# Optimization experiments

Measured on AMD Instinct MI355X. Metric: run time of the kernel, lower is better.

## Reference

```python
import jax, jax.numpy as jnp
import numpy as np

B, LQ, LK, D, H = 8, 1024, 1024, 1024, 16
HD = D // H  # 64


def setup_inputs() -> dict:
    key = jax.random.key(0)
    ks = jax.random.split(key, 8)
    s = 0.02  # weight init scale
    return {
        "q_in": jax.random.normal(ks[0], (B, LQ, D), jnp.float32),
        "k_in": jax.random.normal(ks[1], (B, LK, D), jnp.float32),
        "v_in": jax.random.normal(ks[2], (B, LK, D), jnp.float32),
        "wq": jax.random.normal(ks[3], (D, D), jnp.float32) * s,
        "bq": jnp.zeros((D,), jnp.float32),
        "wk": jax.random.normal(ks[4], (D, D), jnp.float32) * s,
        "bk": jnp.zeros((D,), jnp.float32),
        "wv": jax.random.normal(ks[5], (D, D), jnp.float32) * s,
        "bv": jnp.zeros((D,), jnp.float32),
        "wo": jax.random.normal(ks[6], (D, D), jnp.float32) * s,
        "bo": jnp.zeros((D,), jnp.float32),
        # is_masked=True buffer: tril of ones -> True on lower triangle (masked-out positions, per original masked_fill semantics)
        "mask": jnp.tril(jnp.ones((LQ, LK), jnp.bool_)),
    }


def reference(q_in, k_in, v_in, wq, bq, wk, bk, wv, bv, wo, bo, mask):
    # torch Linear: x @ W.T + b
    q = (q_in @ wq.T + bq).reshape(B, H, LQ, HD)  # plain view, as in original
    k = (k_in @ wk.T + bk).reshape(B, H, LK, HD)
    v = (v_in @ wv.T + bv).reshape(B, H, LK, HD)
    # QUIRK: original scales by sqrt(query.size(1)) == sqrt(head_num), not sqrt(head_dim)
    scale = jnp.sqrt(jnp.float32(H))
    h = jnp.einsum("bhik,bhjk->bhij", q, k) / scale  # [B,H,LQ,LK]
    # masked_fill(-inf) then nan_to_num (maps -inf -> finfo.min, matching torch defaults)
    h = jnp.nan_to_num(jnp.where(mask, -jnp.inf, h))
    w = jax.nn.softmax(h, axis=-1)
    heads = jnp.einsum("bhij,bhjv->bhiv", w, v).reshape(B, LQ, H * HD)
    return heads @ wo.T + bo
```

## Files before the change

kernel.cpp:

```cpp
#include <hip/hip_runtime.h>
#include <hip/hip_bf16.h>

typedef __bf16 bf16;
typedef __attribute__((ext_vector_type(8))) __bf16 bf16x8;
typedef __attribute__((ext_vector_type(4))) float f32x4;

#define BB 8
#define SEQ 1024
#define DD 1024
#define HDIM 64
#define CHUNK 65536
#define MROWS (BB * SEQ)
#define NE_IN 8388608
#define NE_W  1048576

__device__ __forceinline__ void async_load16(const bf16* g, bf16* l) {
  __builtin_amdgcn_global_load_lds(
      (const __attribute__((address_space(1))) void*)g,
      (__attribute__((address_space(3))) void*)l, 16, 0, 0);
}

struct CvtArgs {
  const float* src[7];
  bf16* dst[7];
  int n[7];
};
__global__ __launch_bounds__(256) void cvt_bf16(CvtArgs a) {
  const int t = blockIdx.y;
  const long idx = ((long)blockIdx.x * 256 + threadIdx.x) * 8;
  if (idx >= a.n[t]) return;
  const float* s = a.src[t] + idx;
  f32x4 x = *(const f32x4*)s;
  f32x4 y = *(const f32x4*)(s + 4);
  bf16x8 o;
  o[0] = (bf16)x[0]; o[1] = (bf16)x[1]; o[2] = (bf16)x[2]; o[3] = (bf16)x[3];
  o[4] = (bf16)y[0]; o[5] = (bf16)y[1]; o[6] = (bf16)y[2]; o[7] = (bf16)y[3];
  *(bf16x8*)(a.dst[t] + idx) = o;
}

__global__ __launch_bounds__(256) void gemm_qkv(
    const bf16* __restrict__ Abase, const bf16* __restrict__ Wbase,
    const float* __restrict__ bq, const float* __restrict__ bk,
    const float* __restrict__ bv, bf16* __restrict__ Obase)
{
  __shared__ __attribute__((aligned(16))) bf16 As[128 * 32];
  __shared__ __attribute__((aligned(16))) bf16 Bs[128 * 32];

  const int tid  = threadIdx.x;
  const int lane = tid & 63;
  const int wid  = tid >> 6;
  const int wm   = wid >> 1, wn = wid & 1;
  const int quad = lane >> 4, l15 = lane & 15;
  const int m0 = blockIdx.y * 128;
  const int n0 = blockIdx.x * 128;
  const int t  = n0 >> 10;

  const bf16* A = Abase + (size_t)t * NE_IN;
  const float* bias = (t == 0) ? bq : (t == 1) ? bk : bv;
  const float scale = (t == 0) ? 0.25f : 1.0f;
  bf16* Cout = Obase + (size_t)t * NE_IN;
  const int nc0 = n0 & 1023;

  f32x4 acc[4][4];
#pragma unroll
  for (int i = 0; i < 4; i++)
#pragma unroll
    for (int j = 0; j < 4; j++) acc[i][j] = f32x4{0.f, 0.f, 0.f, 0.f};

  const int srow = wid * 16 + (lane >> 2);
  const int scol = (lane & 3) * 8;
  const bf16* gA = A + (size_t)(m0 + srow) * DD + scol;
  const bf16* gB = Wbase + (size_t)(n0 + srow) * DD + scol;
  bf16* lA = As + wid * 512;
  bf16* lB = Bs + wid * 512;

  for (int k0 = 0; k0 < DD; k0 += 32) {
    async_load16(gA + k0,           lA);
    async_load16(gA + k0 + 64 * DD, lA + 2048);
    async_load16(gB + k0,           lB);
    async_load16(gB + k0 + 64 * DD, lB + 2048);
    __syncthreads();

    bf16x8 af[4], bfr[4];
#pragma unroll
    for (int mi = 0; mi < 4; mi++)
      af[mi] = *(const bf16x8*)&As[(wm * 64 + mi * 16 + l15) * 32 + quad * 8];
#pragma unroll
    for (int ni = 0; ni < 4; ni++)
      bfr[ni] = *(const bf16x8*)&Bs[(wn * 64 + ni * 16 + l15) * 32 + quad * 8];
#pragma unroll
    for (int mi = 0; mi < 4; mi++)
#pragma unroll
      for (int ni = 0; ni < 4; ni++)
        acc[mi][ni] = __builtin_amdgcn_mfma_f32_16x16x32_bf16(
            af[mi], bfr[ni], acc[mi][ni], 0, 0, 0);
    __syncthreads();
  }

#pragma unroll
  for (int mi = 0; mi < 4; mi++) {
#pragma unroll
    for (int ni = 0; ni < 4; ni++) {
      const int col = nc0 + wn * 64 + ni * 16 + l15;
      const float bv_ = bias[col];
#pragma unroll
      for (int r = 0; r < 4; r++) {
        const int row = m0 + wm * 64 + mi * 16 + quad * 4 + r;
        Cout[(size_t)row * DD + col] = (bf16)((acc[mi][ni][r] + bv_) * scale);
      }
    }
  }
}

__global__ __launch_bounds__(256) void gemm_out(
    const bf16* __restrict__ A, const bf16* __restrict__ Bw,
    const float* __restrict__ bias, float* __restrict__ Cout)
{
  __shared__ __attribute__((aligned(16))) bf16 As[128 * 32];
  __shared__ __attribute__((aligned(16))) bf16 Bs[128 * 32];

  const int tid  = threadIdx.x;
  const int lane = tid & 63;
  const int wid  = tid >> 6;
  const int wm   = wid >> 1, wn = wid & 1;
  const int quad = lane >> 4, l15 = lane & 15;
  const int m0 = blockIdx.y * 128;
  const int n0 = blockIdx.x * 128;

  f32x4 acc[4][4];
#pragma unroll
  for (int i = 0; i < 4; i++)
#pragma unroll
    for (int j = 0; j < 4; j++) acc[i][j] = f32x4{0.f, 0.f, 0.f, 0.f};

  const int srow = wid * 16 + (lane >> 2);
  const int scol = (lane & 3) * 8;
  const bf16* gA = A  + (size_t)(m0 + srow) * DD + scol;
  const bf16* gB = Bw + (size_t)(n0 + srow) * DD + scol;
  bf16* lA = As + wid * 512;
  bf16* lB = Bs + wid * 512;

  for (int k0 = 0; k0 < DD; k0 += 32) {
    async_load16(gA + k0,           lA);
    async_load16(gA + k0 + 64 * DD, lA + 2048);
    async_load16(gB + k0,           lB);
    async_load16(gB + k0 + 64 * DD, lB + 2048);
    __syncthreads();

    bf16x8 af[4], bfr[4];
#pragma unroll
    for (int mi = 0; mi < 4; mi++)
      af[mi] = *(const bf16x8*)&As[(wm * 64 + mi * 16 + l15) * 32 + quad * 8];
#pragma unroll
    for (int ni = 0; ni < 4; ni++)
      bfr[ni] = *(const bf16x8*)&Bs[(wn * 64 + ni * 16 + l15) * 32 + quad * 8];
#pragma unroll
    for (int mi = 0; mi < 4; mi++)
#pragma unroll
      for (int ni = 0; ni < 4; ni++)
        acc[mi][ni] = __builtin_amdgcn_mfma_f32_16x16x32_bf16(
            af[mi], bfr[ni], acc[mi][ni], 0, 0, 0);
    __syncthreads();
  }

#pragma unroll
  for (int mi = 0; mi < 4; mi++) {
#pragma unroll
    for (int ni = 0; ni < 4; ni++) {
      const int col = n0 + wn * 64 + ni * 16 + l15;
      const float bv_ = bias[col];
#pragma unroll
      for (int r = 0; r < 4; r++) {
        const int row = m0 + wm * 64 + mi * 16 + quad * 4 + r;
        Cout[(size_t)row * DD + col] = acc[mi][ni][r] + bv_;
      }
    }
  }
}

__global__ __launch_bounds__(256) void vtrans(
    const bf16* __restrict__ V, bf16* __restrict__ Vt)
{
  __shared__ __attribute__((aligned(16))) bf16 T[64][72];
  const int tid = threadIdx.x;
  const int r  = tid >> 2;
  const int c0 = (tid & 3) * 16;
  const size_t base = (size_t)blockIdx.y * CHUNK;
  const int kv0 = blockIdx.x * 64;

  const bf16* src = V + base + (size_t)(kv0 + r) * HDIM + c0;
  *(bf16x8*)&T[r][c0]     = *(const bf16x8*)src;
  *(bf16x8*)&T[r][c0 + 8] = *(const bf16x8*)(src + 8);
  __syncthreads();

  bf16x8 o0, o1;
#pragma unroll
  for (int j = 0; j < 8; j++) { o0[j] = T[c0 + j][r]; o1[j] = T[c0 + 8 + j][r]; }
  bf16* dst = Vt + base + (size_t)r * SEQ + kv0 + c0;
  *(bf16x8*)dst       = o0;
  *(bf16x8*)(dst + 8) = o1;
}

__global__ __launch_bounds__(256) void attn3(
    const bf16* __restrict__ Q, const bf16* __restrict__ K,
    const bf16* __restrict__ Vt, bf16* __restrict__ O)
{
  __shared__ __attribute__((aligned(16))) bf16 Ks[64][72];
  __shared__ __attribute__((aligned(16))) bf16 Vs[64][72];
  __shared__ __attribute__((aligned(16))) bf16 Ps[4][16][72];

  const int tid  = threadIdx.x;
  const int lane = tid & 63;
  const int wid  = tid >> 6;
  const int quad = lane >> 4, l15 = lane & 15;
  const int q0   = blockIdx.y * 64;
  const size_t base = (size_t)blockIdx.x * CHUNK;
  const int qrow0 = q0 + wid * 16;
  const int rowq  = qrow0 + quad * 4;

  bf16x8 qa[2];
#pragma unroll
  for (int ks = 0; ks < 2; ks++)
    qa[ks] = *(const bf16x8*)&Q[base + (size_t)(qrow0 + l15) * HDIM + ks * 32 + quad * 8];

  f32x4 oacc[4];
  float lsum[4] = {0.f, 0.f, 0.f, 0.f};
#pragma unroll
  for (int t = 0; t < 4; t++) oacc[t] = f32x4{0.f, 0.f, 0.f, 0.f};

  const int sr = tid >> 2;
  const int sc = (tid & 3) * 16;
  const bf16* gK = K  + base + (size_t)sr * HDIM + sc;
  const bf16* gV = Vt + base + (size_t)sr * SEQ  + sc;

  const int kv_begin = (q0 == SEQ - 64) ? 0 : q0;

  for (int kv0 = kv_begin; kv0 < SEQ; kv0 += 64) {
    {
      const bf16* pk = gK + (size_t)kv0 * HDIM;
      *(bf16x8*)&Ks[sr][sc]     = *(const bf16x8*)pk;
      *(bf16x8*)&Ks[sr][sc + 8] = *(const bf16x8*)(pk + 8);
      const bf16* pv = gV + kv0;
      *(bf16x8*)&Vs[sr][sc]     = *(const bf16x8*)pv;
      *(bf16x8*)&Vs[sr][sc + 8] = *(const bf16x8*)(pv + 8);
    }
    __syncthreads();

    f32x4 s[4];
#pragma unroll
    for (int ni = 0; ni < 4; ni++) {
      f32x4 a = f32x4{0.f, 0.f, 0.f, 0.f};
#pragma unroll
      for (int ks = 0; ks < 2; ks++) {
        bf16x8 kf = *(const bf16x8*)&Ks[ni * 16 + l15][ks * 32 + quad * 8];
        a = __builtin_amdgcn_mfma_f32_16x16x32_bf16(qa[ks], kf, a, 0, 0, 0);
      }
      s[ni] = a;
    }

#pragma unroll
    for (int ni = 0; ni < 4; ni++) {
      const int kvg = kv0 + ni * 16 + l15;
#pragma unroll
      for (int r = 0; r < 4; r++) {
        const int qg = rowq + r;
        float p;
        if (kvg <= qg) p = (qg == SEQ - 1) ? 1.0f : 0.0f;
        else           p = __expf(s[ni][r]);
        lsum[r] += p;
        Ps[wid][quad * 4 + r][ni * 16 + l15] = (bf16)p;
      }
    }

#pragma unroll
    for (int ks = 0; ks < 2; ks++) {
      bf16x8 pa = *(const bf16x8*)&Ps[wid][l15][ks * 32 + quad * 8];
#pragma unroll
      for (int t = 0; t < 4; t++) {
        bf16x8 vf = *(const bf16x8*)&Vs[t * 16 + l15][ks * 32 + quad * 8];
        oacc[t] = __builtin_amdgcn_mfma_f32_16x16x32_bf16(pa, vf, oacc[t], 0, 0, 0);
      }
    }
    __syncthreads();
  }

  float rinv[4];
#pragma unroll
  for (int r = 0; r < 4; r++) {
    float t = lsum[r];
#pragma unroll
    for (int off = 1; off < 16; off <<= 1) t += __shfl_xor(t, off);
    rinv[r] = 1.0f / t;
  }
#pragma unroll
  for (int t = 0; t < 4; t++)
#pragma unroll
    for (int r = 0; r < 4; r++)
      O[base + (size_t)(rowq + r) * HDIM + t * 16 + l15] = (bf16)(oacc[t][r] * rinv[r]);
}

extern "C" void kernel_launch(void* const* d_in, const int* in_sizes, int n_in,
                              void* d_out, int out_size, void* d_ws, size_t ws_size,
                              hipStream_t stream) {
  (void)in_sizes; (void)n_in; (void)out_size; (void)ws_size;
  const float* q_in = (const float*)d_in[0];
  const float* k_in = (const float*)d_in[1];
  const float* v_in = (const float*)d_in[2];
  const float* wq   = (const float*)d_in[3];
  const float* bq   = (const float*)d_in[4];
  const float* wk   = (const float*)d_in[5];
  const float* bk   = (const float*)d_in[6];
  const float* wv   = (const float*)d_in[7];
  const float* bv   = (const float*)d_in[8];
  const float* wo   = (const float*)d_in[9];
  const float* bo   = (const float*)d_in[10];

  bf16* wqb  = (bf16*)d_ws;
  bf16* wkb  = wqb + NE_W;
  bf16* wvb  = wkb + NE_W;
  bf16* wob  = wvb + NE_W;
  bf16* qinb = wob + NE_W;
  bf16* kinb = qinb + NE_IN;
  bf16* vinb = kinb + NE_IN;
  bf16* Qb   = vinb + NE_IN;
  bf16* Kb   = Qb + NE_IN;
  bf16* Vb   = Kb + NE_IN;
  bf16* VtG  = qinb;
  bf16* Hb   = kinb;

  CvtArgs ca;
  ca.src[0] = q_in; ca.dst[0] = qinb; ca.n[0] = NE_IN;
  ca.src[1] = k_in; ca.dst[1] = kinb; ca.n[1] = NE_IN;
  ca.src[2] = v_in; ca.dst[2] = vinb; ca.n[2] = NE_IN;
  ca.src[3] = wq;   ca.dst[3] = wqb;  ca.n[3] = NE_W;
  ca.src[4] = wk;   ca.dst[4] = wkb;  ca.n[4] = NE_W;
  ca.src[5] = wv;   ca.dst[5] = wvb;  ca.n[5] = NE_W;
  ca.src[6] = wo;   ca.dst[6] = wob;  ca.n[6] = NE_W;
  cvt_bf16<<<dim3(NE_IN / 2048, 7), 256, 0, stream>>>(ca);

  gemm_qkv<<<dim3(3 * DD / 128, MROWS / 128), 256, 0, stream>>>(
      qinb, wqb, bq, bk, bv, Qb);

  vtrans<<<dim3(SEQ / 64, BB * 16), 256, 0, stream>>>(Vb, VtG);
  attn3<<<dim3(BB * 16, SEQ / 64), 256, 0, stream>>>(Qb, Kb, VtG, Hb);

  gemm_out<<<dim3(DD / 128, MROWS / 128), 256, 0, stream>>>(
      Hb, wob, bo, (float*)d_out);
}
```

Measured before the change: 336.5 us.

## Keep attention probabilities in registers via transposed S and fp16 PV MFMA

The attention kernel now computes S transposed (K as the A operand), so each lane's score values line up directly as the B operand of a 16x16x16 fp16 MFMA for P·V. This removes the shared-memory round trip for P and the per-tile cross-lane row-sum reduction. V is stored transposed in fp16 to match, and the output is staged through shared memory for coalesced stores. Separately, the GEMM grid axes are swapped so blockIdx.x walks M tiles, which changes the tile traversal order and L2 reuse. fp16 P and V lower the accumulation precision somewhat, and PV now issues more, smaller MFMAs.

Measured after the change: 331.2 us. About the same (-1.6%).

```diff
diff --git a/kernel.cpp b/kernel.cpp
--- a/kernel.cpp
+++ b/kernel.cpp
@@ -2,7 +2,11 @@
 #include <hip/hip_bf16.h>
 
 typedef __bf16 bf16;
+typedef _Float16 f16;
 typedef __attribute__((ext_vector_type(8))) __bf16 bf16x8;
+typedef __attribute__((ext_vector_type(4))) __bf16 bf16x4;
+typedef __attribute__((ext_vector_type(8))) _Float16 f16x8;
+typedef __attribute__((ext_vector_type(4))) _Float16 f16x4;
 typedef __attribute__((ext_vector_type(4))) float f32x4;
 
 #define BB 8
@@ -51,8 +55,8 @@
   const int wid  = tid >> 6;
   const int wm   = wid >> 1, wn = wid & 1;
   const int quad = lane >> 4, l15 = lane & 15;
-  const int m0 = blockIdx.y * 128;
-  const int n0 = blockIdx.x * 128;
+  const int m0 = blockIdx.x * 128;
+  const int n0 = blockIdx.y * 128;
   const int t  = n0 >> 10;
 
   const bf16* A = Abase + (size_t)t * NE_IN;
@@ -124,8 +128,8 @@
   const int wid  = tid >> 6;
   const int wm   = wid >> 1, wn = wid & 1;
   const int quad = lane >> 4, l15 = lane & 15;
-  const int m0 = blockIdx.y * 128;
-  const int n0 = blockIdx.x * 128;
+  const int m0 = blockIdx.x * 128;
+  const int n0 = blockIdx.y * 128;
 
   f32x4 acc[4][4];
 #pragma unroll
@@ -179,7 +183,7 @@
 }
 
 __global__ __launch_bounds__(256) void vtrans(
-    const bf16* __restrict__ V, bf16* __restrict__ Vt)
+    const bf16* __restrict__ V, f16* __restrict__ Vt)
 {
   __shared__ __attribute__((aligned(16))) bf16 T[64][72];
   const int tid = threadIdx.x;
@@ -193,21 +197,23 @@
   *(bf16x8*)&T[r][c0 + 8] = *(const bf16x8*)(src + 8);
   __syncthreads();
 
-  bf16x8 o0, o1;
-#pragma unroll
-  for (int j = 0; j < 8; j++) { o0[j] = T[c0 + j][r]; o1[j] = T[c0 + 8 + j][r]; }
-  bf16* dst = Vt + base + (size_t)r * SEQ + kv0 + c0;
-  *(bf16x8*)dst       = o0;
-  *(bf16x8*)(dst + 8) = o1;
-}
-
-__global__ __launch_bounds__(256) void attn3(
+  f16x8 o0, o1;
+#pragma unroll
+  for (int j = 0; j < 8; j++) {
+    o0[j] = (f16)(float)T[c0 + j][r];
+    o1[j] = (f16)(float)T[c0 + 8 + j][r];
+  }
+  f16* dst = Vt + base + (size_t)r * SEQ + kv0 + c0;
+  *(f16x8*)dst       = o0;
+  *(f16x8*)(dst + 8) = o1;
+}
+
+__global__ __launch_bounds__(256) void attn5(
     const bf16* __restrict__ Q, const bf16* __restrict__ K,
-    const bf16* __restrict__ Vt, bf16* __restrict__ O)
+    const f16* __restrict__ Vt, bf16* __restrict__ O)
 {
   __shared__ __attribute__((aligned(16))) bf16 Ks[64][72];
-  __shared__ __attribute__((aligned(16))) bf16 Vs[64][72];
-  __shared__ __attribute__((aligned(16))) bf16 Ps[4][16][72];
+  __shared__ __attribute__((aligned(16))) f16  Vs[64][72];
 
   const int tid  = threadIdx.x;
   const int lane = tid & 63;
@@ -215,23 +221,22 @@
   const int quad = lane >> 4, l15 = lane & 15;
   const int q0   = blockIdx.y * 64;
   const size_t base = (size_t)blockIdx.x * CHUNK;
-  const int qrow0 = q0 + wid * 16;
-  const int rowq  = qrow0 + quad * 4;
-
-  bf16x8 qa[2];
+  const int qg = q0 + wid * 16 + l15;
+
+  bf16x8 qb[2];
 #pragma unroll
   for (int ks = 0; ks < 2; ks++)
-    qa[ks] = *(const bf16x8*)&Q[base + (size_t)(qrow0 + l15) * HDIM + ks * 32 + quad * 8];
+    qb[ks] = *(const bf16x8*)&Q[base + (size_t)qg * HDIM + ks * 32 + quad * 8];
 
   f32x4 oacc[4];
-  float lsum[4] = {0.f, 0.f, 0.f, 0.f};
-#pragma unroll
-  for (int t = 0; t < 4; t++) oacc[t] = f32x4{0.f, 0.f, 0.f, 0.f};
+#pragma unroll
+  for (int h = 0; h < 4; h++) oacc[h] = f32x4{0.f, 0.f, 0.f, 0.f};
+  float lsum = 0.f;
 
   const int sr = tid >> 2;
   const int sc = (tid & 3) * 16;
-  const bf16* gK = K  + base + (size_t)sr * HDIM + sc;
-  const bf16* gV = Vt + base + (size_t)sr * SEQ  + sc;
+  const bf16* gK = K + base + (size_t)sr * HDIM + sc;
+  const f16*  gV = Vt + base + (size_t)sr * SEQ + sc;
 
   const int kv_begin = (q0 == SEQ - 64) ? 0 : q0;
 
@@ -240,63 +245,59 @@
       const bf16* pk = gK + (size_t)kv0 * HDIM;
       *(bf16x8*)&Ks[sr][sc]     = *(const bf16x8*)pk;
       *(bf16x8*)&Ks[sr][sc + 8] = *(const bf16x8*)(pk + 8);
-      const bf16* pv = gV + kv0;
-      *(bf16x8*)&Vs[sr][sc]     = *(const bf16x8*)pv;
-      *(bf16x8*)&Vs[sr][sc + 8] = *(const bf16x8*)(pv + 8);
+      const f16* pv = gV + kv0;
+      *(f16x8*)&Vs[sr][sc]     = *(const f16x8*)pv;
+      *(f16x8*)&Vs[sr][sc + 8] = *(const f16x8*)(pv + 8);
     }
     __syncthreads();
 
-    f32x4 s[4];
-#pragma unroll
-    for (int ni = 0; ni < 4; ni++) {
-      f32x4 a = f32x4{0.f, 0.f, 0.f, 0.f};
+#pragma unroll
+    for (int t = 0; t < 4; t++) {
+      f32x4 s = f32x4{0.f, 0.f, 0.f, 0.f};
 #pragma unroll
       for (int ks = 0; ks < 2; ks++) {
-        bf16x8 kf = *(const bf16x8*)&Ks[ni * 16 + l15][ks * 32 + quad * 8];
-        a = __builtin_amdgcn_mfma_f32_16x16x32_bf16(qa[ks], kf, a, 0, 0, 0);
-      }
-      s[ni] = a;
-    }
-
-#pragma unroll
-    for (int ni = 0; ni < 4; ni++) {
-      const int kvg = kv0 + ni * 16 + l15;
+        bf16x8 kf = *(const bf16x8*)&Ks[t * 16 + l15][ks * 32 + quad * 8];
+        s = __builtin_amdgcn_mfma_f32_16x16x32_bf16(kf, qb[ks], s, 0, 0, 0);
+      }
+      f16x4 pf;
 #pragma unroll
       for (int r = 0; r < 4; r++) {
-        const int qg = rowq + r;
+        const int kvg = kv0 + t * 16 + quad * 4 + r;
         float p;
         if (kvg <= qg) p = (qg == SEQ - 1) ? 1.0f : 0.0f;
-        else           p = __expf(s[ni][r]);
-        lsum[r] += p;
-        Ps[wid][quad * 4 + r][ni * 16 + l15] = (bf16)p;
+        else           p = __expf(s[r]);
+        const f16 ph = (f16)p;
+        pf[r] = ph;
+        lsum += (float)ph;
+      }
+#pragma unroll
+      for (int h = 0; h < 4; h++) {
+        f16x4 vf = *(const f16x4*)&Vs[h * 16 + l15][t * 16 + quad * 4];
+        oacc[h] = __builtin_amdgcn_mfma_f32_16x16x16f16(vf, pf, oacc[h], 0, 0, 0);
       }
     }
-
-#pragma unroll
-    for (int ks = 0; ks < 2; ks++) {
-      bf16x8 pa = *(const bf16x8*)&Ps[wid][l15][ks * 32 + quad * 8];
-#pragma unroll
-      for (int t = 0; t < 4; t++) {
-        bf16x8 vf = *(const bf16x8*)&Vs[t * 16 + l15][ks * 32 + quad * 8];
-        oacc[t] = __builtin_amdgcn_mfma_f32_16x16x32_bf16(pa, vf, oacc[t], 0, 0, 0);
-      }
-    }
-    __syncthreads();
-  }
-
-  float rinv[4];
-#pragma unroll
-  for (int r = 0; r < 4; r++) {
-    float t = lsum[r];
-#pragma unroll
-    for (int off = 1; off < 16; off <<= 1) t += __shfl_xor(t, off);
-    rinv[r] = 1.0f / t;
-  }
-#pragma unroll
-  for (int t = 0; t < 4; t++)
-#pragma unroll
-    for (int r = 0; r < 4; r++)
-      O[base + (size_t)(rowq + r) * HDIM + t * 16 + l15] = (bf16)(oacc[t][r] * rinv[r]);
+    __syncthreads();
+  }
+
+  lsum += __shfl_xor(lsum, 16);
+  lsum += __shfl_xor(lsum, 32);
+  const float rinv = 1.0f / lsum;
+
+#pragma unroll
+  for (int h = 0; h < 4; h++) {
+    bf16x4 w;
+#pragma unroll
+    for (int r = 0; r < 4; r++) w[r] = (bf16)(oacc[h][r] * rinv);
+    *(bf16x4*)&Ks[wid * 16 + l15][h * 16 + quad * 4] = w;
+  }
+  __syncthreads();
+  {
+    const int row = tid >> 2;
+    const int c   = (tid & 3) * 16;
+    bf16* dst = O + base + (size_t)(q0 + row) * HDIM + c;
+    *(bf16x8*)dst       = *(const bf16x8*)&Ks[row][c];
+    *(bf16x8*)(dst + 8) = *(const bf16x8*)&Ks[row][c + 8];
+  }
 }
 
 extern "C" void kernel_launch(void* const* d_in, const int* in_sizes, int n_in,
@@ -325,7 +326,7 @@
   bf16* Qb   = vinb + NE_IN;
   bf16* Kb   = Qb + NE_IN;
   bf16* Vb   = Kb + NE_IN;
-  bf16* VtG  = qinb;
+  f16*  VtG  = (f16*)qinb;
   bf16* Hb   = kinb;
 
   CvtArgs ca;
@@ -338,12 +339,12 @@
   ca.src[6] = wo;   ca.dst[6] = wob;  ca.n[6] = NE_W;
   cvt_bf16<<<dim3(NE_IN / 2048, 7), 256, 0, stream>>>(ca);
 
-  gemm_qkv<<<dim3(3 * DD / 128, MROWS / 128), 256, 0, stream>>>(
+  gemm_qkv<<<dim3(MROWS / 128, 3 * DD / 128), 256, 0, stream>>>(
       qinb, wqb, bq, bk, bv, Qb);
 
   vtrans<<<dim3(SEQ / 64, BB * 16), 256, 0, stream>>>(Vb, VtG);
-  attn3<<<dim3(BB * 16, SEQ / 64), 256, 0, stream>>>(Qb, Kb, VtG, Hb);
-
-  gemm_out<<<dim3(DD / 128, MROWS / 128), 256, 0, stream>>>(
+  attn5<<<dim3(BB * 16, SEQ / 64), 256, 0, stream>>>(Qb, Kb, VtG, Hb);
+
+  gemm_out<<<dim3(MROWS / 128, DD / 128), 256, 0, stream>>>(
       Hb, wob, bo, (float*)d_out);
 }
```
